# Performance work log

Hardware: AMD Instinct MI355X
Metric: run time of the kernel (lower is better)

Reference implementation:

```python
import jax, jax.numpy as jnp
import numpy as np

D_MODEL = 1024
NUM_HEADS = 16
D_K = D_MODEL // NUM_HEADS


def setup_inputs() -> dict:
    key = jax.random.key(0)
    ks = jax.random.split(key, 11)
    B, S = 2, 2048
    scale = 1.0 / np.sqrt(D_MODEL)
    inp = {
        "q": jax.random.normal(ks[0], (B, S, D_MODEL), jnp.float32),
        "k": jax.random.normal(ks[1], (B, S, D_MODEL), jnp.float32),
        "v": jax.random.normal(ks[2], (B, S, D_MODEL), jnp.float32),
        "wq_w": jax.random.normal(ks[3], (D_MODEL, D_MODEL), jnp.float32) * scale,
        "wq_b": jnp.zeros((D_MODEL,), jnp.float32),
        "wk_w": jax.random.normal(ks[4], (D_MODEL, D_MODEL), jnp.float32) * scale,
        "wk_b": jnp.zeros((D_MODEL,), jnp.float32),
        "wv_w": jax.random.normal(ks[5], (D_MODEL, D_MODEL), jnp.float32) * scale,
        "wv_b": jnp.zeros((D_MODEL,), jnp.float32),
        "wo_w": jax.random.normal(ks[6], (D_MODEL, D_MODEL), jnp.float32) * scale,
        "wo_b": jnp.zeros((D_MODEL,), jnp.float32),
    }
    return inp


def reference(q, k, v, wq_w, wq_b, wk_w, wk_b, wv_w, wv_b, wo_w, wo_b):
    B, S, _ = q.shape
    H, dk = NUM_HEADS, D_K
    # projections (torch Linear: x @ W.T + b); reshape to [B, H, S, dk]
    qh = (q @ wq_w.T + wq_b).reshape(B, S, H, dk).transpose(0, 2, 1, 3)
    kh = (k @ wk_w.T + wk_b).reshape(B, S, H, dk).transpose(0, 2, 1, 3)
    vh = (v @ wv_w.T + wv_b).reshape(B, S, H, dk).transpose(0, 2, 1, 3)
    # explicit [B,H,S,S] scores, softmax over keys
    scores = jnp.einsum('bhqd,bhkd->bhqk', qh, kh) / np.sqrt(dk).astype(jnp.float32)
    weights = jax.nn.softmax(scores, axis=-1)
    out = jnp.einsum('bhqk,bhkd->bhqd', weights, vh)
    out = out.transpose(0, 2, 1, 3).reshape(B, S, H * dk)
    return out @ wo_w.T + wo_b
```

## Files before the change

### kernel.cpp

```cpp
#include <hip/hip_runtime.h>

#define B_  2
#define S_  2048
#define D_  1024
#define H_  16
#define DK_ 64

typedef __bf16 bf16;
typedef __bf16 bf16x8 __attribute__((ext_vector_type(8)));
typedef __bf16 bf16x4 __attribute__((ext_vector_type(4)));
typedef float  f32x4  __attribute__((ext_vector_type(4)));

#define GLD16(gptr, lptr) __builtin_amdgcn_global_load_lds( \
    (const __attribute__((address_space(1))) void*)(gptr),  \
    (__attribute__((address_space(3))) void*)(lptr), 16, 0, 0)

__global__ __launch_bounds__(256) void cast_all(
    const float* __restrict__ q, const float* __restrict__ k, const float* __restrict__ v,
    const float* __restrict__ wq, const float* __restrict__ wk, const float* __restrict__ wv,
    const float* __restrict__ wo,
    bf16* __restrict__ qb, bf16* __restrict__ kb, bf16* __restrict__ vb,
    bf16* __restrict__ wqb, bf16* __restrict__ wkb, bf16* __restrict__ wvb,
    bf16* __restrict__ wob) {
  int blk = blockIdx.x;
  const float* in; bf16* out; int base;
  if      (blk < 2048) { in = q;  out = qb;  base = blk; }
  else if (blk < 4096) { in = k;  out = kb;  base = blk - 2048; }
  else if (blk < 6144) { in = v;  out = vb;  base = blk - 4096; }
  else if (blk < 6656) { in = wq; out = wqb; base = blk - 6144; }
  else if (blk < 7168) { in = wk; out = wkb; base = blk - 6656; }
  else if (blk < 7680) { in = wv; out = wvb; base = blk - 7168; }
  else                 { in = wo; out = wob; base = blk - 7680; }
  int i = (base * 256 + threadIdx.x) * 8;
  float4 a = *(const float4*)(in + i);
  float4 b = *(const float4*)(in + i + 4);
  bf16x8 o;
  o[0] = (bf16)a.x; o[1] = (bf16)a.y; o[2] = (bf16)a.z; o[3] = (bf16)a.w;
  o[4] = (bf16)b.x; o[5] = (bf16)b.y; o[6] = (bf16)b.z; o[7] = (bf16)b.w;
  *(bf16x8*)(out + i) = o;
}

__global__ __launch_bounds__(256) void gemm_qkv(
    const bf16* __restrict__ qb, const bf16* __restrict__ kb, const bf16* __restrict__ vb,
    const bf16* __restrict__ wq, const bf16* __restrict__ wk, const bf16* __restrict__ wv,
    const float* __restrict__ biq, const float* __restrict__ bik, const float* __restrict__ biv,
    bf16* __restrict__ Qh, bf16* __restrict__ Kh, bf16* __restrict__ Vt) {
  __shared__ bf16 As[128 * 32];
  __shared__ bf16 Bs[128 * 32];
  const int z = blockIdx.y;
  const bf16 *A, *Bm; const float* bias; bf16* Cout;
  int bx, by, N;
  if (z == 0)      { A = qb; Bm = wq; bias = biq; Cout = Qh; }
  else if (z == 1) { A = kb; Bm = wk; bias = bik; Cout = Kh; }
  else             { A = wv; Bm = vb; bias = biv; Cout = Vt; }
  if (z < 2) { bx = blockIdx.x & 7;  by = blockIdx.x >> 3; N = D_; }
  else       { bx = blockIdx.x & 31; by = blockIdx.x >> 5; N = B_ * S_; }
  const int K = D_;

  const int tid  = threadIdx.x;
  const int wave = tid >> 6, lane = tid & 63;
  const int g = lane >> 4, r = lane & 15;
  const int wm = wave >> 1, wn = wave & 1;
  const int m0 = by * 128, n0 = bx * 128;

  f32x4 acc[4][4] = {};
  const int srow = tid >> 2;
  const int sp   = tid & 3;

  for (int k0 = 0; k0 < K; k0 += 32) {
    __syncthreads();
#pragma unroll
    for (int rep = 0; rep < 2; rep++) {
      int row = rep * 64 + srow;
      int bb  = sp ^ ((row >> 1) & 3);
      GLD16(A  + (size_t)(m0 + row) * K + k0 + bb * 8, As + (rep * 256 + wave * 64) * 8);
      GLD16(Bm + (size_t)(n0 + row) * K + k0 + bb * 8, Bs + (rep * 256 + wave * 64) * 8);
    }
    __syncthreads();

    bf16x8 af[4], bfr[4];
#pragma unroll
    for (int i = 0; i < 4; i++) {
      int row = wm * 64 + i * 16 + r;
      af[i] = *(const bf16x8*)(As + row * 32 + (g ^ ((row >> 1) & 3)) * 8);
    }
#pragma unroll
    for (int j = 0; j < 4; j++) {
      int row = wn * 64 + j * 16 + r;
      bfr[j] = *(const bf16x8*)(Bs + row * 32 + (g ^ ((row >> 1) & 3)) * 8);
    }
#pragma unroll
    for (int i = 0; i < 4; i++)
#pragma unroll
      for (int j = 0; j < 4; j++)
        acc[i][j] = __builtin_amdgcn_mfma_f32_16x16x32_bf16(af[i], bfr[j], acc[i][j], 0, 0, 0);
  }

#pragma unroll
  for (int i = 0; i < 4; i++) {
#pragma unroll
    for (int j = 0; j < 4; j++) {
#pragma unroll
      for (int t = 0; t < 4; t++) {
        int mrow = m0 + wm * 64 + i * 16 + g * 4 + t;
        int col  = n0 + wn * 64 + j * 16 + r;
        float val = acc[i][j][t];
        if (z < 2) {
          val += bias[col];
          int bb2 = mrow >> 11, s = mrow & (S_ - 1);
          int hh = col >> 6, d = col & 63;
          Cout[(((size_t)(bb2 * H_ + hh)) * S_ + s) * 64 + d] = (bf16)val;
        } else {
          val += bias[mrow];
          Cout[(size_t)mrow * N + col] = (bf16)val;
        }
      }
    }
  }
}

__global__ __launch_bounds__(256) void gemm_out(const bf16* __restrict__ A,
                                                const bf16* __restrict__ Bm,
                                                const float* __restrict__ bias,
                                                float* __restrict__ Cout) {
  __shared__ bf16 As[128 * 32];
  __shared__ bf16 Bs[64 * 32];
  const int K = D_, N = D_;
  const int tid  = threadIdx.x;
  const int wave = tid >> 6, lane = tid & 63;
  const int g = lane >> 4, r = lane & 15;
  const int m0 = blockIdx.y * 128, n0 = blockIdx.x * 64;

  f32x4 acc[2][4] = {};
  const int srow = tid >> 2;
  const int sp   = tid & 3;

  for (int k0 = 0; k0 < K; k0 += 32) {
    __syncthreads();
#pragma unroll
    for (int rep = 0; rep < 2; rep++) {
      int row = rep * 64 + srow;
      int bb  = sp ^ ((row >> 1) & 3);
      GLD16(A + (size_t)(m0 + row) * K + k0 + bb * 8, As + (rep * 256 + wave * 64) * 8);
    }
    {
      int row = srow;
      int bb  = sp ^ ((row >> 1) & 3);
      GLD16(Bm + (size_t)(n0 + row) * K + k0 + bb * 8, Bs + (wave * 64) * 8);
    }
    __syncthreads();

    bf16x8 af[2], bfr[4];
#pragma unroll
    for (int i = 0; i < 2; i++) {
      int row = wave * 32 + i * 16 + r;
      af[i] = *(const bf16x8*)(As + row * 32 + (g ^ ((row >> 1) & 3)) * 8);
    }
#pragma unroll
    for (int j = 0; j < 4; j++) {
      int row = j * 16 + r;
      bfr[j] = *(const bf16x8*)(Bs + row * 32 + (g ^ ((row >> 1) & 3)) * 8);
    }
#pragma unroll
    for (int i = 0; i < 2; i++)
#pragma unroll
      for (int j = 0; j < 4; j++)
        acc[i][j] = __builtin_amdgcn_mfma_f32_16x16x32_bf16(af[i], bfr[j], acc[i][j], 0, 0, 0);
  }

#pragma unroll
  for (int i = 0; i < 2; i++)
#pragma unroll
    for (int j = 0; j < 4; j++)
#pragma unroll
      for (int t = 0; t < 4; t++) {
        int mrow = m0 + wave * 32 + i * 16 + g * 4 + t;
        int col  = n0 + j * 16 + r;
        Cout[(size_t)mrow * N + col] = acc[i][j][t] + bias[col];
      }
}

__global__ __launch_bounds__(256, 4) void flash_attn(const bf16* __restrict__ Qh,
                                                     const bf16* __restrict__ Kh,
                                                     const bf16* __restrict__ Vt,
                                                     bf16* __restrict__ Apart,
                                                     float* __restrict__ Lpart) {
  __shared__ bf16 Ks[64 * 64];
  __shared__ bf16 Vs[64 * 64];
  __shared__ bf16 Ps[128 * 72];

  const int tid  = threadIdx.x;
  const int wave = tid >> 6, lane = tid & 63;
  const int g = lane >> 4, r = lane & 15;

  int qt = blockIdx.x & 15;
  int kh = (blockIdx.x >> 4) & 1;
  int bh = blockIdx.x >> 5;
  int h = bh & (H_ - 1), b = bh >> 4;

  const bf16* Kbase = Kh + ((size_t)bh * S_ + kh * 1024) * DK_;
  const bf16* Vbase = Vt + (size_t)h * 64 * (B_ * S_) + (size_t)b * S_ + kh * 1024;

  bf16x8 bq[2][2];
#pragma unroll
  for (int sq = 0; sq < 2; sq++) {
    int qrow = qt * 128 + wave * 32 + sq * 16 + r;
    const bf16* qp = Qh + ((size_t)bh * S_ + qrow) * DK_;
#pragma unroll
    for (int kc = 0; kc < 2; kc++)
      bq[sq][kc] = *(const bf16x8*)(qp + kc * 32 + g * 8);
  }

  f32x4 acc_o[2][4] = {};
  float l_run[2] = {0.f, 0.f};
  const float sc2 = 0.18033688f;

  const int srow = tid >> 3, spp = tid & 7;

  for (int j0 = 0; j0 < 1024 / 64; j0++) {
    __syncthreads();
#pragma unroll
    for (int rep = 0; rep < 2; rep++) {
      int rr = rep * 32 + srow;
      int bb = spp ^ (rr & 7);
      GLD16(Kbase + (size_t)(j0 * 64 + rr) * 64 + bb * 8, Ks + (rep * 256 + wave * 64) * 8);
      GLD16(Vbase + (size_t)rr * (B_ * S_) + j0 * 64 + bb * 8, Vs + (rep * 256 + wave * 64) * 8);
    }
    __syncthreads();

    bf16x8 ak[4][2];
#pragma unroll
    for (int ks = 0; ks < 4; ks++) {
      int kr = ks * 16 + r;
#pragma unroll
      for (int kc = 0; kc < 2; kc++)
        ak[ks][kc] = *(const bf16x8*)(Ks + kr * 64 + (((kc * 4 + g) ^ (kr & 7)) * 8));
    }
    f32x4 sacc[2][4] = {};
#pragma unroll
    for (int sq = 0; sq < 2; sq++)
#pragma unroll
      for (int ks = 0; ks < 4; ks++)
#pragma unroll
        for (int kc = 0; kc < 2; kc++)
          sacc[sq][ks] = __builtin_amdgcn_mfma_f32_16x16x32_bf16(ak[ks][kc], bq[sq][kc],
                                                                 sacc[sq][ks], 0, 0, 0);

#pragma unroll
    for (int sq = 0; sq < 2; sq++) {
      int qrow = wave * 32 + sq * 16 + r;
      float rs = 0.f;
#pragma unroll
      for (int ks = 0; ks < 4; ks++) {
        bf16x4 pk;
#pragma unroll
        for (int t = 0; t < 4; t++) {
          float pv = __builtin_amdgcn_exp2f(sacc[sq][ks][t] * sc2);
          rs += pv;
          pk[t] = (bf16)pv;
        }
        *(bf16x4*)(Ps + qrow * 72 + ks * 16 + g * 4) = pk;
      }
      l_run[sq] += rs;
    }

    asm volatile("s_waitcnt lgkmcnt(0)" ::: "memory");

    bf16x8 bp[2][2];
#pragma unroll
    for (int sq = 0; sq < 2; sq++) {
      int qrow = wave * 32 + sq * 16 + r;
#pragma unroll
      for (int kc2 = 0; kc2 < 2; kc2++)
        bp[sq][kc2] = *(const bf16x8*)(Ps + qrow * 72 + kc2 * 32 + g * 8);
    }
#pragma unroll
    for (int dsub = 0; dsub < 4; dsub++) {
      int dr = dsub * 16 + r;
      bf16x8 av[2];
#pragma unroll
      for (int kc2 = 0; kc2 < 2; kc2++)
        av[kc2] = *(const bf16x8*)(Vs + dr * 64 + (((kc2 * 4 + g) ^ (r & 7)) * 8));
#pragma unroll
      for (int sq = 0; sq < 2; sq++)
#pragma unroll
        for (int kc2 = 0; kc2 < 2; kc2++)
          acc_o[sq][dsub] = __builtin_amdgcn_mfma_f32_16x16x32_bf16(av[kc2], bp[sq][kc2],
                                                                    acc_o[sq][dsub], 0, 0, 0);
    }
  }

#pragma unroll
  for (int sq = 0; sq < 2; sq++) {
    float l = l_run[sq];
    l += __shfl_xor(l, 16, 64);
    l += __shfl_xor(l, 32, 64);
    int s = qt * 128 + wave * 32 + sq * 16 + r;
    if (g == 0)
      Lpart[(size_t)kh * (B_ * H_ * S_) + (size_t)bh * S_ + s] = l;
    size_t base = (size_t)kh * (B_ * S_ * (size_t)D_) + ((size_t)b * S_ + s) * D_ + (size_t)h * 64;
#pragma unroll
    for (int dsub = 0; dsub < 4; dsub++) {
      bf16x4 o;
#pragma unroll
      for (int t = 0; t < 4; t++) o[t] = (bf16)(acc_o[sq][dsub][t]);
      *(bf16x4*)(Apart + base + dsub * 16 + g * 4) = o;
    }
  }
}

__global__ __launch_bounds__(256) void combine(const bf16* __restrict__ Apart,
                                               const float* __restrict__ Lpart,
                                               bf16* __restrict__ AO) {
  const size_t EQ = (size_t)B_ * S_ * D_;
  const int LHALF = B_ * H_ * S_;
  int idx = (blockIdx.x * 256 + threadIdx.x) * 8;
  int token = idx >> 10;
  int dcol  = idx & (D_ - 1);
  int b = token >> 11, s = token & (S_ - 1);
  int h = dcol >> 6;
  int li = (b * H_ + h) * S_ + s;
  float inv = 1.0f / (Lpart[li] + Lpart[li + LHALF]);
  bf16x8 a0 = *(const bf16x8*)(Apart + idx);
  bf16x8 a1 = *(const bf16x8*)(Apart + EQ + idx);
  bf16x8 o;
#pragma unroll
  for (int t = 0; t < 8; t++) o[t] = (bf16)(((float)a0[t] + (float)a1[t]) * inv);
  *(bf16x8*)(AO + idx) = o;
}

extern "C" void kernel_launch(void* const* d_in, const int* in_sizes, int n_in,
                              void* d_out, int out_size, void* d_ws, size_t ws_size,
                              hipStream_t stream) {
  const float* q    = (const float*)d_in[0];
  const float* k    = (const float*)d_in[1];
  const float* v    = (const float*)d_in[2];
  const float* wq_w = (const float*)d_in[3];
  const float* wq_b = (const float*)d_in[4];
  const float* wk_w = (const float*)d_in[5];
  const float* wk_b = (const float*)d_in[6];
  const float* wv_w = (const float*)d_in[7];
  const float* wv_b = (const float*)d_in[8];
  const float* wo_w = (const float*)d_in[9];
  const float* wo_b = (const float*)d_in[10];

  bf16* W = (bf16*)d_ws;
  const size_t NTOK = (size_t)B_ * S_;
  const size_t EQ = NTOK * D_;
  const size_t EW = (size_t)D_ * D_;
  bf16* qb  = W;
  bf16* kb  = qb  + EQ;
  bf16* vb  = kb  + EQ;
  bf16* Qhb = vb  + EQ;
  bf16* Khb = Qhb + EQ;
  bf16* Vtb = Khb + EQ;
  bf16* AOb = Vtb + EQ;
  bf16* wqb = AOb + EQ;
  bf16* wkb = wqb + EW;
  bf16* wvb = wkb + EW;
  bf16* wob = wvb + EW;

  bf16*  Apart = qb;
  float* Lpart = (float*)vb;

  cast_all<<<8192, 256, 0, stream>>>(q, k, v, wq_w, wk_w, wv_w, wo_w,
                                     qb, kb, vb, wqb, wkb, wvb, wob);

  gemm_qkv<<<dim3(256, 3), 256, 0, stream>>>(qb, kb, vb, wqb, wkb, wvb,
                                             wq_b, wk_b, wv_b, Qhb, Khb, Vtb);

  flash_attn<<<1024, 256, 0, stream>>>(Qhb, Khb, Vtb, Apart, Lpart);

  combine<<<2048, 256, 0, stream>>>(Apart, Lpart, AOb);

  gemm_out<<<dim3(D_ / 64, NTOK / 128), 256, 0, stream>>>(AOb, wob, wo_b, (float*)d_out);
}
```

Before: 230.9 us.

## Deepen GEMM K-tiles, split attention keys four ways, fold softmax scale into Q

Both GEMMs now stage 64-wide K tiles in LDS with an 8-way XOR swizzle, so the loop runs half as many iterations and barriers. The softmax scale is applied once to Q in the projection epilogue instead of to every score in the attention kernel. Attention splits the keys into four chunks instead of two, launching twice as many blocks with a smaller P buffer and a higher occupancy hint. The P·V product is now processed in two 32-key halves. Combine reads four partials, and in-place aliasing of AOb as both a partial and the output adds memory traffic and some aliasing risk.

Measured after the change: 533.0 us. 131% more time.

```diff
diff --git a/kernel.cpp b/kernel.cpp
--- a/kernel.cpp
+++ b/kernel.cpp
@@ -45,8 +45,8 @@
     const bf16* __restrict__ wq, const bf16* __restrict__ wk, const bf16* __restrict__ wv,
     const float* __restrict__ biq, const float* __restrict__ bik, const float* __restrict__ biv,
     bf16* __restrict__ Qh, bf16* __restrict__ Kh, bf16* __restrict__ Vt) {
-  __shared__ bf16 As[128 * 32];
-  __shared__ bf16 Bs[128 * 32];
+  __shared__ bf16 As[128 * 64];
+  __shared__ bf16 Bs[128 * 64];
   const int z = blockIdx.y;
   const bf16 *A, *Bm; const float* bias; bf16* Cout;
   int bx, by, N;
@@ -64,38 +64,42 @@
   const int m0 = by * 128, n0 = bx * 128;
 
   f32x4 acc[4][4] = {};
-  const int srow = tid >> 2;
-  const int sp   = tid & 3;
-
-  for (int k0 = 0; k0 < K; k0 += 32) {
-    __syncthreads();
-#pragma unroll
-    for (int rep = 0; rep < 2; rep++) {
-      int row = rep * 64 + srow;
-      int bb  = sp ^ ((row >> 1) & 3);
-      GLD16(A  + (size_t)(m0 + row) * K + k0 + bb * 8, As + (rep * 256 + wave * 64) * 8);
-      GLD16(Bm + (size_t)(n0 + row) * K + k0 + bb * 8, Bs + (rep * 256 + wave * 64) * 8);
-    }
-    __syncthreads();
-
-    bf16x8 af[4], bfr[4];
-#pragma unroll
-    for (int i = 0; i < 4; i++) {
-      int row = wm * 64 + i * 16 + r;
-      af[i] = *(const bf16x8*)(As + row * 32 + (g ^ ((row >> 1) & 3)) * 8);
-    }
-#pragma unroll
-    for (int j = 0; j < 4; j++) {
-      int row = wn * 64 + j * 16 + r;
-      bfr[j] = *(const bf16x8*)(Bs + row * 32 + (g ^ ((row >> 1) & 3)) * 8);
-    }
-#pragma unroll
-    for (int i = 0; i < 4; i++)
-#pragma unroll
-      for (int j = 0; j < 4; j++)
-        acc[i][j] = __builtin_amdgcn_mfma_f32_16x16x32_bf16(af[i], bfr[j], acc[i][j], 0, 0, 0);
-  }
-
+  const int srow = tid >> 3;
+  const int sp   = tid & 7;
+
+  for (int k0 = 0; k0 < K; k0 += 64) {
+    __syncthreads();
+#pragma unroll
+    for (int rep = 0; rep < 4; rep++) {
+      int row = rep * 32 + srow;
+      int bb  = sp ^ (row & 7);
+      GLD16(A  + (size_t)(m0 + row) * K + k0 + bb * 8, As + rep * 2048 + wave * 512);
+      GLD16(Bm + (size_t)(n0 + row) * K + k0 + bb * 8, Bs + rep * 2048 + wave * 512);
+    }
+    __syncthreads();
+
+#pragma unroll
+    for (int kc = 0; kc < 2; kc++) {
+      bf16x8 af[4], bfr[4];
+#pragma unroll
+      for (int i = 0; i < 4; i++) {
+        int row = wm * 64 + i * 16 + r;
+        af[i] = *(const bf16x8*)(As + row * 64 + (((kc * 4 + g) ^ (row & 7)) * 8));
+      }
+#pragma unroll
+      for (int j = 0; j < 4; j++) {
+        int row = wn * 64 + j * 16 + r;
+        bfr[j] = *(const bf16x8*)(Bs + row * 64 + (((kc * 4 + g) ^ (row & 7)) * 8));
+      }
+#pragma unroll
+      for (int i = 0; i < 4; i++)
+#pragma unroll
+        for (int j = 0; j < 4; j++)
+          acc[i][j] = __builtin_amdgcn_mfma_f32_16x16x32_bf16(af[i], bfr[j], acc[i][j], 0, 0, 0);
+    }
+  }
+
+  const float qscale = 0.18033688f;
 #pragma unroll
   for (int i = 0; i < 4; i++) {
 #pragma unroll
@@ -107,6 +111,7 @@
         float val = acc[i][j][t];
         if (z < 2) {
           val += bias[col];
+          if (z == 0) val *= qscale;
           int bb2 = mrow >> 11, s = mrow & (S_ - 1);
           int hh = col >> 6, d = col & 63;
           Cout[(((size_t)(bb2 * H_ + hh)) * S_ + s) * 64 + d] = (bf16)val;
@@ -123,8 +128,8 @@
                                                 const bf16* __restrict__ Bm,
                                                 const float* __restrict__ bias,
                                                 float* __restrict__ Cout) {
-  __shared__ bf16 As[128 * 32];
-  __shared__ bf16 Bs[64 * 32];
+  __shared__ bf16 As[128 * 64];
+  __shared__ bf16 Bs[64 * 64];
   const int K = D_, N = D_;
   const int tid  = threadIdx.x;
   const int wave = tid >> 6, lane = tid & 63;
@@ -132,40 +137,44 @@
   const int m0 = blockIdx.y * 128, n0 = blockIdx.x * 64;
 
   f32x4 acc[2][4] = {};
-  const int srow = tid >> 2;
-  const int sp   = tid & 3;
-
-  for (int k0 = 0; k0 < K; k0 += 32) {
-    __syncthreads();
+  const int srow = tid >> 3;
+  const int sp   = tid & 7;
+
+  for (int k0 = 0; k0 < K; k0 += 64) {
+    __syncthreads();
+#pragma unroll
+    for (int rep = 0; rep < 4; rep++) {
+      int row = rep * 32 + srow;
+      int bb  = sp ^ (row & 7);
+      GLD16(A + (size_t)(m0 + row) * K + k0 + bb * 8, As + rep * 2048 + wave * 512);
+    }
 #pragma unroll
     for (int rep = 0; rep < 2; rep++) {
-      int row = rep * 64 + srow;
-      int bb  = sp ^ ((row >> 1) & 3);
-      GLD16(A + (size_t)(m0 + row) * K + k0 + bb * 8, As + (rep * 256 + wave * 64) * 8);
-    }
-    {
-      int row = srow;
-      int bb  = sp ^ ((row >> 1) & 3);
-      GLD16(Bm + (size_t)(n0 + row) * K + k0 + bb * 8, Bs + (wave * 64) * 8);
-    }
-    __syncthreads();
-
-    bf16x8 af[2], bfr[4];
-#pragma unroll
-    for (int i = 0; i < 2; i++) {
-      int row = wave * 32 + i * 16 + r;
-      af[i] = *(const bf16x8*)(As + row * 32 + (g ^ ((row >> 1) & 3)) * 8);
-    }
-#pragma unroll
-    for (int j = 0; j < 4; j++) {
-      int row = j * 16 + r;
-      bfr[j] = *(const bf16x8*)(Bs + row * 32 + (g ^ ((row >> 1) & 3)) * 8);
-    }
-#pragma unroll
-    for (int i = 0; i < 2; i++)
-#pragma unroll
-      for (int j = 0; j < 4; j++)
-        acc[i][j] = __builtin_amdgcn_mfma_f32_16x16x32_bf16(af[i], bfr[j], acc[i][j], 0, 0, 0);
+      int row = rep * 32 + srow;
+      int bb  = sp ^ (row & 7);
+      GLD16(Bm + (size_t)(n0 + row) * K + k0 + bb * 8, Bs + rep * 2048 + wave * 512);
+    }
+    __syncthreads();
+
+#pragma unroll
+    for (int kc = 0; kc < 2; kc++) {
+      bf16x8 af[2], bfr[4];
+#pragma unroll
+      for (int i = 0; i < 2; i++) {
+        int row = wave * 32 + i * 16 + r;
+        af[i] = *(const bf16x8*)(As + row * 64 + (((kc * 4 + g) ^ (row & 7)) * 8));
+      }
+#pragma unroll
+      for (int j = 0; j < 4; j++) {
+        int row = j * 16 + r;
+        bfr[j] = *(const bf16x8*)(Bs + row * 64 + (((kc * 4 + g) ^ (row & 7)) * 8));
+      }
+#pragma unroll
+      for (int i = 0; i < 2; i++)
+#pragma unroll
+        for (int j = 0; j < 4; j++)
+          acc[i][j] = __builtin_amdgcn_mfma_f32_16x16x32_bf16(af[i], bfr[j], acc[i][j], 0, 0, 0);
+    }
   }
 
 #pragma unroll
@@ -180,26 +189,30 @@
       }
 }
 
-__global__ __launch_bounds__(256, 4) void flash_attn(const bf16* __restrict__ Qh,
+__global__ __launch_bounds__(256, 6) void flash_attn(const bf16* __restrict__ Qh,
                                                      const bf16* __restrict__ Kh,
                                                      const bf16* __restrict__ Vt,
-                                                     bf16* __restrict__ Apart,
+                                                     bf16* __restrict__ A0,
+                                                     bf16* __restrict__ A1,
+                                                     bf16* __restrict__ A2,
+                                                     bf16* __restrict__ A3,
                                                      float* __restrict__ Lpart) {
   __shared__ bf16 Ks[64 * 64];
   __shared__ bf16 Vs[64 * 64];
-  __shared__ bf16 Ps[128 * 72];
+  __shared__ bf16 Ps[128 * 40];
 
   const int tid  = threadIdx.x;
   const int wave = tid >> 6, lane = tid & 63;
   const int g = lane >> 4, r = lane & 15;
 
   int qt = blockIdx.x & 15;
-  int kh = (blockIdx.x >> 4) & 1;
-  int bh = blockIdx.x >> 5;
+  int kh = (blockIdx.x >> 4) & 3;
+  int bh = blockIdx.x >> 6;
   int h = bh & (H_ - 1), b = bh >> 4;
 
-  const bf16* Kbase = Kh + ((size_t)bh * S_ + kh * 1024) * DK_;
-  const bf16* Vbase = Vt + (size_t)h * 64 * (B_ * S_) + (size_t)b * S_ + kh * 1024;
+  const bf16* Kbase = Kh + ((size_t)bh * S_ + kh * 512) * DK_;
+  const bf16* Vbase = Vt + (size_t)h * 64 * (B_ * S_) + (size_t)b * S_ + kh * 512;
+  bf16* Apart = (kh == 0) ? A0 : (kh == 1) ? A1 : (kh == 2) ? A2 : A3;
 
   bf16x8 bq[2][2];
 #pragma unroll
@@ -213,18 +226,17 @@
 
   f32x4 acc_o[2][4] = {};
   float l_run[2] = {0.f, 0.f};
-  const float sc2 = 0.18033688f;
 
   const int srow = tid >> 3, spp = tid & 7;
 
-  for (int j0 = 0; j0 < 1024 / 64; j0++) {
+  for (int j0 = 0; j0 < 512 / 64; j0++) {
     __syncthreads();
 #pragma unroll
     for (int rep = 0; rep < 2; rep++) {
       int rr = rep * 32 + srow;
       int bb = spp ^ (rr & 7);
-      GLD16(Kbase + (size_t)(j0 * 64 + rr) * 64 + bb * 8, Ks + (rep * 256 + wave * 64) * 8);
-      GLD16(Vbase + (size_t)rr * (B_ * S_) + j0 * 64 + bb * 8, Vs + (rep * 256 + wave * 64) * 8);
+      GLD16(Kbase + (size_t)(j0 * 64 + rr) * 64 + bb * 8, Ks + rep * 2048 + wave * 512);
+      GLD16(Vbase + (size_t)rr * (B_ * S_) + j0 * 64 + bb * 8, Vs + rep * 2048 + wave * 512);
     }
     __syncthreads();
 
@@ -247,46 +259,42 @@
                                                                  sacc[sq][ks], 0, 0, 0);
 
 #pragma unroll
-    for (int sq = 0; sq < 2; sq++) {
-      int qrow = wave * 32 + sq * 16 + r;
-      float rs = 0.f;
-#pragma unroll
-      for (int ks = 0; ks < 4; ks++) {
-        bf16x4 pk;
-#pragma unroll
-        for (int t = 0; t < 4; t++) {
-          float pv = __builtin_amdgcn_exp2f(sacc[sq][ks][t] * sc2);
-          rs += pv;
-          pk[t] = (bf16)pv;
+    for (int c = 0; c < 2; c++) {
+#pragma unroll
+      for (int sq = 0; sq < 2; sq++) {
+        int qrow = wave * 32 + sq * 16 + r;
+        float rs = 0.f;
+#pragma unroll
+        for (int k2 = 0; k2 < 2; k2++) {
+          int ks = c * 2 + k2;
+          bf16x4 pk;
+#pragma unroll
+          for (int t = 0; t < 4; t++) {
+            float pv = __builtin_amdgcn_exp2f(sacc[sq][ks][t]);
+            rs += pv;
+            pk[t] = (bf16)pv;
+          }
+          *(bf16x4*)(Ps + qrow * 40 + k2 * 16 + g * 4) = pk;
         }
-        *(bf16x4*)(Ps + qrow * 72 + ks * 16 + g * 4) = pk;
-      }
-      l_run[sq] += rs;
-    }
-
-    asm volatile("s_waitcnt lgkmcnt(0)" ::: "memory");
-
-    bf16x8 bp[2][2];
-#pragma unroll
-    for (int sq = 0; sq < 2; sq++) {
-      int qrow = wave * 32 + sq * 16 + r;
-#pragma unroll
-      for (int kc2 = 0; kc2 < 2; kc2++)
-        bp[sq][kc2] = *(const bf16x8*)(Ps + qrow * 72 + kc2 * 32 + g * 8);
-    }
-#pragma unroll
-    for (int dsub = 0; dsub < 4; dsub++) {
-      int dr = dsub * 16 + r;
-      bf16x8 av[2];
-#pragma unroll
-      for (int kc2 = 0; kc2 < 2; kc2++)
-        av[kc2] = *(const bf16x8*)(Vs + dr * 64 + (((kc2 * 4 + g) ^ (r & 7)) * 8));
-#pragma unroll
-      for (int sq = 0; sq < 2; sq++)
-#pragma unroll
-        for (int kc2 = 0; kc2 < 2; kc2++)
-          acc_o[sq][dsub] = __builtin_amdgcn_mfma_f32_16x16x32_bf16(av[kc2], bp[sq][kc2],
+        l_run[sq] += rs;
+      }
+      asm volatile("s_waitcnt lgkmcnt(0)" ::: "memory");
+
+      bf16x8 bp[2];
+#pragma unroll
+      for (int sq = 0; sq < 2; sq++) {
+        int qrow = wave * 32 + sq * 16 + r;
+        bp[sq] = *(const bf16x8*)(Ps + qrow * 40 + g * 8);
+      }
+#pragma unroll
+      for (int dsub = 0; dsub < 4; dsub++) {
+        int dr = dsub * 16 + r;
+        bf16x8 av = *(const bf16x8*)(Vs + dr * 64 + (((c * 4 + g) ^ (dr & 7)) * 8));
+#pragma unroll
+        for (int sq = 0; sq < 2; sq++)
+          acc_o[sq][dsub] = __builtin_amdgcn_mfma_f32_16x16x32_bf16(av, bp[sq],
                                                                     acc_o[sq][dsub], 0, 0, 0);
+      }
     }
   }
 
@@ -298,7 +306,7 @@
     int s = qt * 128 + wave * 32 + sq * 16 + r;
     if (g == 0)
       Lpart[(size_t)kh * (B_ * H_ * S_) + (size_t)bh * S_ + s] = l;
-    size_t base = (size_t)kh * (B_ * S_ * (size_t)D_) + ((size_t)b * S_ + s) * D_ + (size_t)h * 64;
+    size_t base = ((size_t)b * S_ + s) * D_ + (size_t)h * 64;
 #pragma unroll
     for (int dsub = 0; dsub < 4; dsub++) {
       bf16x4 o;
@@ -309,10 +317,10 @@
   }
 }
 
-__global__ __launch_bounds__(256) void combine(const bf16* __restrict__ Apart,
+__global__ __launch_bounds__(256) void combine(const bf16* a0, const bf16* a1,
+                                               const bf16* a2, const bf16* a3,
                                                const float* __restrict__ Lpart,
-                                               bf16* __restrict__ AO) {
-  const size_t EQ = (size_t)B_ * S_ * D_;
+                                               bf16* AO) {
   const int LHALF = B_ * H_ * S_;
   int idx = (blockIdx.x * 256 + threadIdx.x) * 8;
   int token = idx >> 10;
@@ -320,12 +328,15 @@
   int b = token >> 11, s = token & (S_ - 1);
   int h = dcol >> 6;
   int li = (b * H_ + h) * S_ + s;
-  float inv = 1.0f / (Lpart[li] + Lpart[li + LHALF]);
-  bf16x8 a0 = *(const bf16x8*)(Apart + idx);
-  bf16x8 a1 = *(const bf16x8*)(Apart + EQ + idx);
+  float inv = 1.0f / (Lpart[li] + Lpart[li + LHALF] + Lpart[li + 2 * LHALF] + Lpart[li + 3 * LHALF]);
+  bf16x8 x0 = *(const bf16x8*)(a0 + idx);
+  bf16x8 x1 = *(const bf16x8*)(a1 + idx);
+  bf16x8 x2 = *(const bf16x8*)(a2 + idx);
+  bf16x8 x3 = *(const bf16x8*)(a3 + idx);
   bf16x8 o;
 #pragma unroll
-  for (int t = 0; t < 8; t++) o[t] = (bf16)(((float)a0[t] + (float)a1[t]) * inv);
+  for (int t = 0; t < 8; t++)
+    o[t] = (bf16)((((float)x0[t] + (float)x1[t]) + ((float)x2[t] + (float)x3[t])) * inv);
   *(bf16x8*)(AO + idx) = o;
 }
 
@@ -360,8 +371,7 @@
   bf16* wvb = wkb + EW;
   bf16* wob = wvb + EW;
 
-  bf16*  Apart = qb;
-  float* Lpart = (float*)vb;
+  float* Lpart = (float*)wqb;
 
   cast_all<<<8192, 256, 0, stream>>>(q, k, v, wq_w, wk_w, wv_w, wo_w,
                                      qb, kb, vb, wqb, wkb, wvb, wob);
@@ -369,9 +379,9 @@
   gemm_qkv<<<dim3(256, 3), 256, 0, stream>>>(qb, kb, vb, wqb, wkb, wvb,
                                              wq_b, wk_b, wv_b, Qhb, Khb, Vtb);
 
-  flash_attn<<<1024, 256, 0, stream>>>(Qhb, Khb, Vtb, Apart, Lpart);
-
-  combine<<<2048, 256, 0, stream>>>(Apart, Lpart, AOb);
+  flash_attn<<<2048, 256, 0, stream>>>(Qhb, Khb, Vtb, qb, kb, vb, AOb, Lpart);
+
+  combine<<<2048, 256, 0, stream>>>(qb, kb, vb, AOb, Lpart, AOb);
 
   gemm_out<<<dim3(D_ / 64, NTOK / 128), 256, 0, stream>>>(AOb, wob, wo_b, (float*)d_out);
 }
```

## Shrink QKV GEMM tiles, fold softmax scale into Q, split P·V in halves

Applied to the files above, without the earlier changes.

The QKV projection GEMM moves from 128x128 to 128x64 tiles, doubling the grid and adding an occupancy hint of 6 blocks per CU. The softmax scale constant is folded into the Q projection epilogue, so flash attention no longer multiplies every score. Flash attention now writes and consumes P in two 32-key halves, which shrinks the P shared buffer, and its block index mapping is reordered so neighbouring blocks share Q and K/V data. Smaller tiles lower per-block reuse, and folding the scale before the bf16 rounding of Q slightly changes numerics.

Result: no change. 229.4 us (-0.7%).

```diff
diff --git a/kernel.cpp b/kernel.cpp
--- a/kernel.cpp
+++ b/kernel.cpp
@@ -40,30 +40,29 @@
   *(bf16x8*)(out + i) = o;
 }
 
-__global__ __launch_bounds__(256) void gemm_qkv(
+__global__ __launch_bounds__(256, 6) void gemm_qkv(
     const bf16* __restrict__ qb, const bf16* __restrict__ kb, const bf16* __restrict__ vb,
     const bf16* __restrict__ wq, const bf16* __restrict__ wk, const bf16* __restrict__ wv,
     const float* __restrict__ biq, const float* __restrict__ bik, const float* __restrict__ biv,
     bf16* __restrict__ Qh, bf16* __restrict__ Kh, bf16* __restrict__ Vt) {
   __shared__ bf16 As[128 * 32];
-  __shared__ bf16 Bs[128 * 32];
+  __shared__ bf16 Bs[64 * 32];
   const int z = blockIdx.y;
   const bf16 *A, *Bm; const float* bias; bf16* Cout;
   int bx, by, N;
   if (z == 0)      { A = qb; Bm = wq; bias = biq; Cout = Qh; }
   else if (z == 1) { A = kb; Bm = wk; bias = bik; Cout = Kh; }
   else             { A = wv; Bm = vb; bias = biv; Cout = Vt; }
-  if (z < 2) { bx = blockIdx.x & 7;  by = blockIdx.x >> 3; N = D_; }
-  else       { bx = blockIdx.x & 31; by = blockIdx.x >> 5; N = B_ * S_; }
+  if (z < 2) { by = blockIdx.x & 31; bx = blockIdx.x >> 5; N = D_; }
+  else       { bx = blockIdx.x & 63; by = blockIdx.x >> 6; N = B_ * S_; }
   const int K = D_;
 
   const int tid  = threadIdx.x;
   const int wave = tid >> 6, lane = tid & 63;
   const int g = lane >> 4, r = lane & 15;
-  const int wm = wave >> 1, wn = wave & 1;
-  const int m0 = by * 128, n0 = bx * 128;
-
-  f32x4 acc[4][4] = {};
+  const int m0 = by * 128, n0 = bx * 64;
+
+  f32x4 acc[2][4] = {};
   const int srow = tid >> 2;
   const int sp   = tid & 3;
 
@@ -73,40 +72,46 @@
     for (int rep = 0; rep < 2; rep++) {
       int row = rep * 64 + srow;
       int bb  = sp ^ ((row >> 1) & 3);
-      GLD16(A  + (size_t)(m0 + row) * K + k0 + bb * 8, As + (rep * 256 + wave * 64) * 8);
-      GLD16(Bm + (size_t)(n0 + row) * K + k0 + bb * 8, Bs + (rep * 256 + wave * 64) * 8);
-    }
-    __syncthreads();
-
-    bf16x8 af[4], bfr[4];
-#pragma unroll
-    for (int i = 0; i < 4; i++) {
-      int row = wm * 64 + i * 16 + r;
+      GLD16(A + (size_t)(m0 + row) * K + k0 + bb * 8, As + (rep * 256 + wave * 64) * 8);
+    }
+    {
+      int row = srow;
+      int bb  = sp ^ ((row >> 1) & 3);
+      GLD16(Bm + (size_t)(n0 + row) * K + k0 + bb * 8, Bs + (wave * 64) * 8);
+    }
+    __syncthreads();
+
+    bf16x8 af[2], bfr[4];
+#pragma unroll
+    for (int i = 0; i < 2; i++) {
+      int row = wave * 32 + i * 16 + r;
       af[i] = *(const bf16x8*)(As + row * 32 + (g ^ ((row >> 1) & 3)) * 8);
     }
 #pragma unroll
     for (int j = 0; j < 4; j++) {
-      int row = wn * 64 + j * 16 + r;
+      int row = j * 16 + r;
       bfr[j] = *(const bf16x8*)(Bs + row * 32 + (g ^ ((row >> 1) & 3)) * 8);
     }
 #pragma unroll
-    for (int i = 0; i < 4; i++)
+    for (int i = 0; i < 2; i++)
 #pragma unroll
       for (int j = 0; j < 4; j++)
         acc[i][j] = __builtin_amdgcn_mfma_f32_16x16x32_bf16(af[i], bfr[j], acc[i][j], 0, 0, 0);
   }
 
-#pragma unroll
-  for (int i = 0; i < 4; i++) {
+  const float qscale = 0.18033688f;
+#pragma unroll
+  for (int i = 0; i < 2; i++) {
 #pragma unroll
     for (int j = 0; j < 4; j++) {
 #pragma unroll
       for (int t = 0; t < 4; t++) {
-        int mrow = m0 + wm * 64 + i * 16 + g * 4 + t;
-        int col  = n0 + wn * 64 + j * 16 + r;
+        int mrow = m0 + wave * 32 + i * 16 + g * 4 + t;
+        int col  = n0 + j * 16 + r;
         float val = acc[i][j][t];
         if (z < 2) {
           val += bias[col];
+          if (z == 0) val *= qscale;
           int bb2 = mrow >> 11, s = mrow & (S_ - 1);
           int hh = col >> 6, d = col & 63;
           Cout[(((size_t)(bb2 * H_ + hh)) * S_ + s) * 64 + d] = (bf16)val;
@@ -187,15 +192,15 @@
                                                      float* __restrict__ Lpart) {
   __shared__ bf16 Ks[64 * 64];
   __shared__ bf16 Vs[64 * 64];
-  __shared__ bf16 Ps[128 * 72];
+  __shared__ bf16 Ps[128 * 40];
 
   const int tid  = threadIdx.x;
   const int wave = tid >> 6, lane = tid & 63;
   const int g = lane >> 4, r = lane & 15;
 
-  int qt = blockIdx.x & 15;
-  int kh = (blockIdx.x >> 4) & 1;
-  int bh = blockIdx.x >> 5;
+  int qt = blockIdx.x >> 6;
+  int kh = blockIdx.x & 1;
+  int bh = (blockIdx.x >> 1) & 31;
   int h = bh & (H_ - 1), b = bh >> 4;
 
   const bf16* Kbase = Kh + ((size_t)bh * S_ + kh * 1024) * DK_;
@@ -213,7 +218,6 @@
 
   f32x4 acc_o[2][4] = {};
   float l_run[2] = {0.f, 0.f};
-  const float sc2 = 0.18033688f;
 
   const int srow = tid >> 3, spp = tid & 7;
 
@@ -223,8 +227,8 @@
     for (int rep = 0; rep < 2; rep++) {
       int rr = rep * 32 + srow;
       int bb = spp ^ (rr & 7);
-      GLD16(Kbase + (size_t)(j0 * 64 + rr) * 64 + bb * 8, Ks + (rep * 256 + wave * 64) * 8);
-      GLD16(Vbase + (size_t)rr * (B_ * S_) + j0 * 64 + bb * 8, Vs + (rep * 256 + wave * 64) * 8);
+      GLD16(Kbase + (size_t)(j0 * 64 + rr) * 64 + bb * 8, Ks + rep * 2048 + wave * 512);
+      GLD16(Vbase + (size_t)rr * (B_ * S_) + j0 * 64 + bb * 8, Vs + rep * 2048 + wave * 512);
     }
     __syncthreads();
 
@@ -247,46 +251,42 @@
                                                                  sacc[sq][ks], 0, 0, 0);
 
 #pragma unroll
-    for (int sq = 0; sq < 2; sq++) {
-      int qrow = wave * 32 + sq * 16 + r;
-      float rs = 0.f;
-#pragma unroll
-      for (int ks = 0; ks < 4; ks++) {
-        bf16x4 pk;
-#pragma unroll
-        for (int t = 0; t < 4; t++) {
-          float pv = __builtin_amdgcn_exp2f(sacc[sq][ks][t] * sc2);
-          rs += pv;
-          pk[t] = (bf16)pv;
+    for (int c = 0; c < 2; c++) {
+#pragma unroll
+      for (int sq = 0; sq < 2; sq++) {
+        int qrow = wave * 32 + sq * 16 + r;
+        float rs = 0.f;
+#pragma unroll
+        for (int k2 = 0; k2 < 2; k2++) {
+          int ks = c * 2 + k2;
+          bf16x4 pk;
+#pragma unroll
+          for (int t = 0; t < 4; t++) {
+            float pv = __builtin_amdgcn_exp2f(sacc[sq][ks][t]);
+            rs += pv;
+            pk[t] = (bf16)pv;
+          }
+          *(bf16x4*)(Ps + qrow * 40 + k2 * 16 + g * 4) = pk;
         }
-        *(bf16x4*)(Ps + qrow * 72 + ks * 16 + g * 4) = pk;
-      }
-      l_run[sq] += rs;
-    }
-
-    asm volatile("s_waitcnt lgkmcnt(0)" ::: "memory");
-
-    bf16x8 bp[2][2];
-#pragma unroll
-    for (int sq = 0; sq < 2; sq++) {
-      int qrow = wave * 32 + sq * 16 + r;
-#pragma unroll
-      for (int kc2 = 0; kc2 < 2; kc2++)
-        bp[sq][kc2] = *(const bf16x8*)(Ps + qrow * 72 + kc2 * 32 + g * 8);
-    }
-#pragma unroll
-    for (int dsub = 0; dsub < 4; dsub++) {
-      int dr = dsub * 16 + r;
-      bf16x8 av[2];
-#pragma unroll
-      for (int kc2 = 0; kc2 < 2; kc2++)
-        av[kc2] = *(const bf16x8*)(Vs + dr * 64 + (((kc2 * 4 + g) ^ (r & 7)) * 8));
-#pragma unroll
-      for (int sq = 0; sq < 2; sq++)
-#pragma unroll
-        for (int kc2 = 0; kc2 < 2; kc2++)
-          acc_o[sq][dsub] = __builtin_amdgcn_mfma_f32_16x16x32_bf16(av[kc2], bp[sq][kc2],
+        l_run[sq] += rs;
+      }
+      asm volatile("s_waitcnt lgkmcnt(0)" ::: "memory");
+
+      bf16x8 bp[2];
+#pragma unroll
+      for (int sq = 0; sq < 2; sq++) {
+        int qrow = wave * 32 + sq * 16 + r;
+        bp[sq] = *(const bf16x8*)(Ps + qrow * 40 + g * 8);
+      }
+#pragma unroll
+      for (int dsub = 0; dsub < 4; dsub++) {
+        int dr = dsub * 16 + r;
+        bf16x8 av = *(const bf16x8*)(Vs + dr * 64 + (((c * 4 + g) ^ (dr & 7)) * 8));
+#pragma unroll
+        for (int sq = 0; sq < 2; sq++)
+          acc_o[sq][dsub] = __builtin_amdgcn_mfma_f32_16x16x32_bf16(av, bp[sq],
                                                                     acc_o[sq][dsub], 0, 0, 0);
+      }
     }
   }
 
@@ -366,7 +366,7 @@
   cast_all<<<8192, 256, 0, stream>>>(q, k, v, wq_w, wk_w, wv_w, wo_w,
                                      qb, kb, vb, wqb, wkb, wvb, wob);
 
-  gemm_qkv<<<dim3(256, 3), 256, 0, stream>>>(qb, kb, vb, wqb, wkb, wvb,
+  gemm_qkv<<<dim3(512, 3), 256, 0, stream>>>(qb, kb, vb, wqb, wkb, wvb,
                                              wq_b, wk_b, wv_b, Qhb, Khb, Vtb);
 
   flash_attn<<<1024, 256, 0, stream>>>(Qhb, Khb, Vtb, Apart, Lpart);
```
